# Performance work log

Hardware: AMD Instinct MI355X
Metric: run time of the kernel (lower is better)

The kernel has to match this reference:

```python
import jax, jax.numpy as jnp
import numpy as np

N_EMB = 1024
E_DIM = 256


def setup_inputs() -> dict:
    key = jax.random.key(0)
    k1, k2 = jax.random.split(key)
    z = jax.random.normal(k1, (32, E_DIM, 64, 64), dtype=jnp.float32)
    # torch init: uniform_(-1/e_dim, 1/e_dim)
    emb = jax.random.uniform(k2, (N_EMB, E_DIM), dtype=jnp.float32,
                             minval=-1.0 / E_DIM, maxval=1.0 / E_DIM)
    return {"z": z, "emb": emb}


def reference(z, emb):
    # z: [bs, c, h, w] -> [bs, h, w, c] -> [N, e_dim]
    zp = jnp.transpose(z, (0, 2, 3, 1))
    zf = zp.reshape(-1, emb.shape[1])
    # squared euclidean distance via ||z||^2 + ||e||^2 - 2 z.e
    z_sq = jnp.sum(zf * zf, axis=1, keepdims=True)          # [N, 1]
    e_sq = jnp.sum(emb * emb, axis=1)                        # [n_emb]
    e_z = jnp.matmul(zf, emb.T)                              # [N, n_emb]
    dist = z_sq + e_sq - 2.0 * e_z
    idx = jnp.argmin(dist, axis=1)                           # [N] int
    z_q = emb[idx].reshape(zp.shape)                         # [bs, h, w, c]
    z_q = jnp.transpose(z_q, (0, 3, 1, 2))                   # [bs, c, h, w]
    return z_q, idx
```

## Files before the change

### kernel.cpp

```cpp
#include <hip/hip_runtime.h>
#include <float.h>

#define NEMB 1024
#define EDIM 256
#define BM   64
#define HW   4096
#define NB   8
#define NT   1024
#define NW   (NT / 64)
#define ZQ_ELEMS 33554432

template <typename F>
__device__ __forceinline__ float np_sumsq_256(F get) {
#pragma clang fp contract(off)
    float blk[2];
#pragma unroll
    for (int h = 0; h < 2; ++h) {
        const int base = h * 128;
        float r[8];
#pragma unroll
        for (int j = 0; j < 8; ++j) {
            float v = get(base + j);
            r[j] = v * v;
        }
        for (int i = 8; i < 128; i += 8) {
#pragma unroll
            for (int j = 0; j < 8; ++j) {
                float v = get(base + i + j);
                float p = v * v;
                r[j] = r[j] + p;
            }
        }
        blk[h] = ((r[0] + r[1]) + (r[2] + r[3])) + ((r[4] + r[5]) + (r[6] + r[7]));
    }
    return blk[0] + blk[1];
}

__global__ __launch_bounds__(256) void esq_kernel(const float* __restrict__ emb,
                                                  float* __restrict__ esq) {
    int n = blockIdx.x * 256 + threadIdx.x;
    const float* e = emb + (size_t)n * EDIM;
    esq[n] = np_sumsq_256([&](int k) { return e[k]; });
}

__global__ __launch_bounds__(NT, 8) void vq_kernel(const float* __restrict__ z,
                                                   const float* __restrict__ emb,
                                                   const float* __restrict__ esq,
                                                   float* __restrict__ out) {
    __shared__ float zl[BM * EDIM];

    const int t   = threadIdx.x;
    const int blk = blockIdx.x;
    const int b   = blk >> 6;
    const int hw0 = (blk & 63) * BM;
    const float* zb = z + (size_t)b * EDIM * HW;

#pragma unroll
    for (int pass = 0; pass < 4; ++pass) {
        int f4 = pass * NT + t;
        int r4 = (f4 & 15) * 4;
        int k  = f4 >> 4;
        float4 v = *(const float4*)(zb + (size_t)k * HW + hw0 + r4);
        *(float4*)(&zl[k * BM + r4]) = v;
    }
    __syncthreads();

    const int r = t & 63;
    const float zsq = np_sumsq_256([&](int k) { return zl[k * BM + r]; });

    const int q = __builtin_amdgcn_readfirstlane(t >> 6);

    float best = FLT_MAX;
    int   bidx = 0;
    for (int n0 = q * 64; n0 < q * 64 + 64; n0 += NB) {
        float acc[NB];
#pragma unroll
        for (int j = 0; j < NB; ++j) acc[j] = 0.f;

        float zk[8], zk2[8];
#pragma unroll
        for (int u = 0; u < 8; ++u) zk[u] = zl[u * BM + r];
        for (int k = 0; k < EDIM; k += 16) {
#pragma unroll
            for (int u = 0; u < 8; ++u) zk2[u] = zl[(k + 8 + u) * BM + r];
#pragma unroll
            for (int j = 0; j < NB; ++j) {
                const float* er = emb + (size_t)(n0 + j) * EDIM + k;
                float a = acc[j];
#pragma unroll
                for (int u = 0; u < 8; ++u) a = fmaf(zk[u], er[u], a);
                acc[j] = a;
            }
            if (k + 16 < EDIM) {
#pragma unroll
                for (int u = 0; u < 8; ++u) zk[u] = zl[(k + 16 + u) * BM + r];
            }
#pragma unroll
            for (int j = 0; j < NB; ++j) {
                const float* er = emb + (size_t)(n0 + j) * EDIM + k + 8;
                float a = acc[j];
#pragma unroll
                for (int u = 0; u < 8; ++u) a = fmaf(zk2[u], er[u], a);
                acc[j] = a;
            }
        }
#pragma unroll
        for (int j = 0; j < NB; ++j) {
            float t1 = zsq + esq[n0 + j];
            float d  = fmaf(-2.f, acc[j], t1);
            if (d < best) { best = d; bidx = n0 + j; }
        }
    }

    __syncthreads();
    float* rv   = zl;
    int*   ri   = (int*)(zl + NT);
    int*   ifin = (int*)(zl + 2 * NT);
    rv[t] = best;
    ri[t] = bidx;
    __syncthreads();
    if (t < 64) {
        float bv = rv[t];
        int   bi = ri[t];
#pragma unroll
        for (int w = 1; w < NW; ++w) {
            float v = rv[t + 64 * w];
            int   i = ri[t + 64 * w];
            if (v < bv) { bv = v; bi = i; }
        }
        ifin[t] = bi;
        out[(size_t)ZQ_ELEMS + (size_t)blk * BM + t] = (float)bi;
    }
    __syncthreads();

    float* zq = out + (size_t)b * EDIM * HW;
#pragma unroll
    for (int pass = 0; pass < 4; ++pass) {
        int f4 = pass * NT + t;
        int r4 = (f4 & 15) * 4;
        int c  = f4 >> 4;
        float4 v;
        v.x = emb[(size_t)ifin[r4 + 0] * EDIM + c];
        v.y = emb[(size_t)ifin[r4 + 1] * EDIM + c];
        v.z = emb[(size_t)ifin[r4 + 2] * EDIM + c];
        v.w = emb[(size_t)ifin[r4 + 3] * EDIM + c];
        *(float4*)(zq + (size_t)c * HW + hw0 + r4) = v;
    }
}

extern "C" void kernel_launch(void* const* d_in, const int* in_sizes, int n_in,
                              void* d_out, int out_size, void* d_ws, size_t ws_size,
                              hipStream_t stream) {
    const float* z   = (const float*)d_in[0];
    const float* emb = (const float*)d_in[1];
    float* out = (float*)d_out;
    float* esq = (float*)d_ws;

    esq_kernel<<<NEMB / 256, 256, 0, stream>>>(emb, esq);
    vq_kernel<<<131072 / BM, NT, 0, stream>>>(z, emb, esq, out);
}
```

Before: 1.369 ms.

## Widen codebook tile to 16 and interleave shared z layout for float2 reads

Each pass now processes 16 codebook rows instead of 8, so every z value loaded from LDS is reused across more accumulators and there are half as many outer iterations. The shared z tile is stored with pairs of channels interleaved, so each thread fetches two channels with one float2 LDS read, and the FMA loop is reordered to go u-outer, j-inner. The trade-off is more registers for accumulators and embedding operands, which may lower occupancy at 1024 threads per block, and the interleaved LDS stores may cause bank conflicts during the tile load.

```diff
diff --git a/kernel.cpp b/kernel.cpp
--- a/kernel.cpp
+++ b/kernel.cpp
@@ -5,7 +5,7 @@
 #define EDIM 256
 #define BM   64
 #define HW   4096
-#define NB   8
+#define NB   16
 #define NT   1024
 #define NW   (NT / 64)
 #define ZQ_ELEMS 33554432
@@ -61,47 +61,64 @@
         int r4 = (f4 & 15) * 4;
         int k  = f4 >> 4;
         float4 v = *(const float4*)(zb + (size_t)k * HW + hw0 + r4);
-        *(float4*)(&zl[k * BM + r4]) = v;
+        int w = (k >> 1) * 128 + 2 * r4 + (k & 1);
+        zl[w + 0] = v.x;
+        zl[w + 2] = v.y;
+        zl[w + 4] = v.z;
+        zl[w + 6] = v.w;
     }
     __syncthreads();
 
     const int r = t & 63;
-    const float zsq = np_sumsq_256([&](int k) { return zl[k * BM + r]; });
+    const float* zr = zl + 2 * r;
+    const float zsq = np_sumsq_256([&](int k) { return zr[(k >> 1) * 128 + (k & 1)]; });
 
     const int q = __builtin_amdgcn_readfirstlane(t >> 6);
 
     float best = FLT_MAX;
     int   bidx = 0;
-    for (int n0 = q * 64; n0 < q * 64 + 64; n0 += NB) {
+#pragma unroll 1
+    for (int g = 0; g < 4; ++g) {
+        const int n0 = q * 64 + g * NB;
         float acc[NB];
 #pragma unroll
         for (int j = 0; j < NB; ++j) acc[j] = 0.f;
 
-        float zk[8], zk2[8];
+        float2 zk[4], zk2[4];
 #pragma unroll
-        for (int u = 0; u < 8; ++u) zk[u] = zl[u * BM + r];
+        for (int u = 0; u < 4; ++u) zk[u] = *(const float2*)(zr + u * 128);
         for (int k = 0; k < EDIM; k += 16) {
 #pragma unroll
-            for (int u = 0; u < 8; ++u) zk2[u] = zl[(k + 8 + u) * BM + r];
+            for (int u = 0; u < 4; ++u)
+                zk2[u] = *(const float2*)(zr + ((k + 8) >> 1) * 128 + u * 128);
 #pragma unroll
-            for (int j = 0; j < NB; ++j) {
-                const float* er = emb + (size_t)(n0 + j) * EDIM + k;
-                float a = acc[j];
+            for (int jh = 0; jh < 2; ++jh) {
+                const float* eb = emb + (size_t)(n0 + jh * 8) * EDIM + k;
 #pragma unroll
-                for (int u = 0; u < 8; ++u) a = fmaf(zk[u], er[u], a);
-                acc[j] = a;
+                for (int u = 0; u < 8; ++u) {
+                    const float zv = (u & 1) ? zk[u >> 1].y : zk[u >> 1].x;
+#pragma unroll
+                    for (int j2 = 0; j2 < 8; ++j2)
+                        acc[jh * 8 + j2] = fmaf(zv, eb[(size_t)j2 * EDIM + u],
+                                                acc[jh * 8 + j2]);
+                }
             }
             if (k + 16 < EDIM) {
 #pragma unroll
-                for (int u = 0; u < 8; ++u) zk[u] = zl[(k + 16 + u) * BM + r];
+                for (int u = 0; u < 4; ++u)
+                    zk[u] = *(const float2*)(zr + ((k + 16) >> 1) * 128 + u * 128);
             }
 #pragma unroll
-            for (int j = 0; j < NB; ++j) {
-                const float* er = emb + (size_t)(n0 + j) * EDIM + k + 8;
-                float a = acc[j];
+            for (int jh = 0; jh < 2; ++jh) {
+                const float* eb = emb + (size_t)(n0 + jh * 8) * EDIM + k + 8;
 #pragma unroll
-                for (int u = 0; u < 8; ++u) a = fmaf(zk2[u], er[u], a);
-                acc[j] = a;
+                for (int u = 0; u < 8; ++u) {
+                    const float zv = (u & 1) ? zk2[u >> 1].y : zk2[u >> 1].x;
+#pragma unroll
+                    for (int j2 = 0; j2 < 8; ++j2)
+                        acc[jh * 8 + j2] = fmaf(zv, eb[(size_t)j2 * EDIM + u],
+                                                acc[jh * 8 + j2]);
+                }
             }
         }
 #pragma unroll
```

After: 1.253 ms. 8.5% less time.

## Widen codebook tile to 16 rows with interleaved LDS z layout and vector loads

Applied to the files above, without the earlier changes.

Doubles the number of codebook rows accumulated per pass (NB 8→16) and relaxes the launch bound to 4 waves per SIMD so more accumulators fit in registers. The z tile in shared memory is re-laid out with adjacent k pairs interleaved, so each thread reads float2 from LDS, and embedding rows are read as float4 through a VGPR-offset pointer (a zero held in a vector register via inline asm) that forces per-lane vector memory loads instead of scalar loads. The intent is fewer LDS reads per FMA and wider global loads for the embedding. The trade is lower occupancy and higher register pressure, with the k loop no longer unrolled.

```diff
diff --git a/kernel.cpp b/kernel.cpp
--- a/kernel.cpp
+++ b/kernel.cpp
@@ -5,9 +5,9 @@
 #define EDIM 256
 #define BM   64
 #define HW   4096
-#define NB   8
 #define NT   1024
 #define NW   (NT / 64)
+#define NB   16
 #define ZQ_ELEMS 33554432
 
 template <typename F>
@@ -43,7 +43,7 @@
     esq[n] = np_sumsq_256([&](int k) { return e[k]; });
 }
 
-__global__ __launch_bounds__(NT, 8) void vq_kernel(const float* __restrict__ z,
+__global__ __launch_bounds__(NT, 4) void vq_kernel(const float* __restrict__ z,
                                                    const float* __restrict__ emb,
                                                    const float* __restrict__ esq,
                                                    float* __restrict__ out) {
@@ -53,57 +53,65 @@
     const int blk = blockIdx.x;
     const int b   = blk >> 6;
     const int hw0 = (blk & 63) * BM;
-    const float* zb = z + (size_t)b * EDIM * HW;
+    const float* zbase = z + (size_t)b * EDIM * HW;
 
 #pragma unroll
     for (int pass = 0; pass < 4; ++pass) {
         int f4 = pass * NT + t;
         int r4 = (f4 & 15) * 4;
         int k  = f4 >> 4;
-        float4 v = *(const float4*)(zb + (size_t)k * HW + hw0 + r4);
-        *(float4*)(&zl[k * BM + r4]) = v;
+        float4 v = *(const float4*)(zbase + (size_t)k * HW + hw0 + r4);
+        int w = (k >> 1) * 128 + 2 * r4 + (k & 1);
+        zl[w + 0] = v.x;
+        zl[w + 2] = v.y;
+        zl[w + 4] = v.z;
+        zl[w + 6] = v.w;
     }
     __syncthreads();
 
     const int r = t & 63;
-    const float zsq = np_sumsq_256([&](int k) { return zl[k * BM + r]; });
+    const float* zr = zl + 2 * r;
+    const float zsq = np_sumsq_256([&](int k) { return zr[(k >> 1) * 128 + (k & 1)]; });
 
     const int q = __builtin_amdgcn_readfirstlane(t >> 6);
 
+    int lzero;
+    asm("v_mov_b32 %0, 0" : "=v"(lzero));
+    const float* embv = emb + lzero;
+
     float best = FLT_MAX;
     int   bidx = 0;
-    for (int n0 = q * 64; n0 < q * 64 + 64; n0 += NB) {
+
+#pragma unroll 1
+    for (int g = 0; g < 4; ++g) {
+        const int n0 = q * 64 + g * NB;
+        const float* p0 = embv + (size_t)n0 * EDIM;
+        const float* p1 = p0 + 4 * EDIM;
+        const float* p2 = p0 + 8 * EDIM;
+        const float* p3 = p0 + 12 * EDIM;
+
         float acc[NB];
 #pragma unroll
         for (int j = 0; j < NB; ++j) acc[j] = 0.f;
 
-        float zk[8], zk2[8];
-#pragma unroll
-        for (int u = 0; u < 8; ++u) zk[u] = zl[u * BM + r];
-        for (int k = 0; k < EDIM; k += 16) {
-#pragma unroll
-            for (int u = 0; u < 8; ++u) zk2[u] = zl[(k + 8 + u) * BM + r];
+#pragma unroll 1
+        for (int kc = 0; kc < EDIM; kc += 4) {
+            const int m0 = kc >> 1;
+            float2 z0 = *(const float2*)(zr + (m0 + 0) * 128);
+            float2 z1 = *(const float2*)(zr + (m0 + 1) * 128);
 #pragma unroll
             for (int j = 0; j < NB; ++j) {
-                const float* er = emb + (size_t)(n0 + j) * EDIM + k;
+                const float* pj = (j < 4) ? p0 : (j < 8) ? p1 : (j < 12) ? p2 : p3;
+                float4 ef = *(const float4*)(pj + (j & 3) * EDIM + kc);
                 float a = acc[j];
-#pragma unroll
-                for (int u = 0; u < 8; ++u) a = fmaf(zk[u], er[u], a);
-                acc[j] = a;
-            }
-            if (k + 16 < EDIM) {
-#pragma unroll
-                for (int u = 0; u < 8; ++u) zk[u] = zl[(k + 16 + u) * BM + r];
-            }
-#pragma unroll
-            for (int j = 0; j < NB; ++j) {
-                const float* er = emb + (size_t)(n0 + j) * EDIM + k + 8;
-                float a = acc[j];
-#pragma unroll
-                for (int u = 0; u < 8; ++u) a = fmaf(zk2[u], er[u], a);
+                a = fmaf(z0.x, ef.x, a);
+                a = fmaf(z0.y, ef.y, a);
+                a = fmaf(z1.x, ef.z, a);
+                a = fmaf(z1.y, ef.w, a);
                 acc[j] = a;
             }
         }
+
 #pragma unroll
         for (int j = 0; j < NB; ++j) {
             float t1 = zsq + esq[n0 + j];
```

New measurement: 3.867 ms. 2.82x slower.
